# Kernel tuning notes

Measured on AMD Instinct MI355X. Metric: run time of the kernel, lower is better.

The kernel has to match this reference:

```python
import jax, jax.numpy as jnp
import numpy as np

BS, S, D, N, E = 16, 8, 10, 32, 300
H, STATE_DIM, MID, OC = 128, 96, 256, 100

def setup_inputs():
    ks = jax.random.split(jax.random.key(0), 24)
    g = lambda i, shape: (0.02 * jax.random.normal(ks[i], shape)).astype(jnp.float32)
    return {
        "stock_news": jax.random.normal(ks[0], (BS, S, D, N, E), dtype=jnp.float32),
        "stock_feats": jax.random.normal(ks[1], (BS, STATE_DIM), dtype=jnp.float32),
        "conv_w3": g(2, (S, OC, E, 3)), "conv_b3": g(3, (S, OC)),
        "conv_w4": g(4, (S, OC, E, 4)), "conv_b4": g(5, (S, OC)),
        "conv_w5": g(6, (S, OC, E, 5)), "conv_b5": g(7, (S, OC)),
        "w_ih": g(8, (S, 4 * H, 3 * OC)), "w_hh": g(9, (S, 4 * H, H)),
        "b_ih": g(10, (S, 4 * H)), "b_hh": g(11, (S, 4 * H)),
        "linX_w": g(12, (S, H, 2 * H)), "linX_b": g(13, (S, H)),
        "linY_w": g(14, (S, 64, H)), "linY_b": g(15, (S, 64)),
        "w1": g(16, (24, STATE_DIM)), "b1": g(17, (24,)),
        "w2": g(18, (16, 24)), "b2": g(19, (16,)),
        "arch_w1": g(20, (MID, 16 + 64 * S)), "arch_b1": g(21, (MID,)),
        "arch_w2": g(22, (S, MID)), "arch_b2": g(23, (S,)),
        "action_var": jnp.full((S,), -0.25, dtype=jnp.float32),
    }

def _conv_maxpool(x, w, b, k):
    # x: [S,B,D,N,E], w: [S,OC,E,k] -> conv1d over news axis then max-pool -> [S,B,D,OC]
    L = x.shape[3] - k + 1
    y = jnp.broadcast_to(b[:, None, None, None, :], (x.shape[0], x.shape[1], x.shape[2], L, w.shape[1]))
    for j in range(k):
        y = y + jnp.einsum('sbdne,soe->sbdno', x[:, :, :, j:j + L, :], w[:, :, :, j])
    return y.max(axis=3)

def _lstm_attn(xs, w_ih, w_hh, b_ih, b_hh):
    # single-stock LSTM (batch_first) + attention from original code; xs: [B,D,I] -> [B,2H]
    pre = jnp.einsum('bdi,gi->dbg', xs, w_ih) + b_ih + b_hh  # [D,B,4H]
    h0 = jnp.zeros((xs.shape[0], w_hh.shape[1]), xs.dtype)
    def step(carry, g_t):
        h, c = carry
        gates = g_t + h @ w_hh.T
        i, f, g, o = jnp.split(gates, 4, axis=-1)  # PyTorch gate order i,f,g,o
        c = jax.nn.sigmoid(f) * c + jax.nn.sigmoid(i) * jnp.tanh(g)
        h = jax.nn.sigmoid(o) * jnp.tanh(c)
        return (h, c), h
    (hn, _), outs = jax.lax.scan(step, (h0, h0), pre)
    outs = outs.transpose(1, 0, 2)  # [B,D,H]
    w = jnp.einsum('bh,bdh->bd', hn, outs)[:, None, :]  # [B,1,D]
    w = jax.nn.softmax(w, axis=1)  # softmax over singleton dim, exactly as torch code (yields ones)
    out = jnp.sum(w.transpose(0, 2, 1) * outs, axis=1)  # [B,H]
    return jnp.concatenate([hn, out], axis=-1)  # [B,2H]

def _forward(stock_news, stock_feats, conv_w3, conv_b3, conv_w4, conv_b4, conv_w5, conv_b5,
             w_ih, w_hh, b_ih, b_hh, linX_w, linX_b, linY_w, linY_b,
             w1, b1, w2, b2, arch_w1, arch_b1, arch_w2, arch_b2, action_var):
    x = stock_news.transpose(1, 0, 2, 3, 4)  # [S,B,D,N,E]
    feats = [_conv_maxpool(x, w, b, k) for (w, b, k) in
             ((conv_w3, conv_b3, 3), (conv_w4, conv_b4, 4), (conv_w5, conv_b5, 5))]
    text = jnp.concatenate(feats, axis=-1)  # [S,B,D,300]
    comb = jax.vmap(_lstm_attn)(text, w_ih, w_hh, b_ih, b_hh)  # [S,B,2H]
    hX = jax.nn.relu(jnp.einsum('sbi,shi->sbh', comb, linX_w) + linX_b[:, None, :])  # dropout is eval-mode identity
    hY = jax.nn.relu(jnp.einsum('sbh,soh->sbo', hX, linY_w) + linY_b[:, None, :])  # [S,B,64]
    stock_text = hY.transpose(1, 0, 2).reshape(stock_news.shape[0], -1)  # [B,S*64]
    f = jax.nn.relu(stock_feats @ w1.T + b1) @ w2.T + b2  # [B,16]
    total = jnp.concatenate([stock_text, f], axis=-1)  # [B,16+64S]
    mu = jnp.tanh(jax.nn.relu(total @ arch_w1.T + arch_b1) @ arch_w2.T + arch_b2)
    return mu, jnp.exp(action_var)

def reference(stock_news, stock_feats, conv_w3, conv_b3, conv_w4, conv_b4, conv_w5, conv_b5,
              w_ih, w_hh, b_ih, b_hh, linX_w, linX_b, linY_w, linY_b,
              w1, b1, w2, b2, arch_w1, arch_b1, arch_w2, arch_b2, action_var):
    return _forward(stock_news, stock_feats, conv_w3, conv_b3, conv_w4, conv_b4, conv_w5, conv_b5,
                    w_ih, w_hh, b_ih, b_hh, linX_w, linX_b, linY_w, linY_b,
                    w1, b1, w2, b2, arch_w1, arch_b1, arch_w2, arch_b2, action_var)
```

## Files before the change

### kernel.cpp

```cpp
#include <hip/hip_runtime.h>
#include <math.h>

#define S_   8
#define B_   16
#define D_   10
#define N_   32
#define E_   300
#define H_   128
#define G4_  512
#define SDIM_ 96
#define MID_ 256
#define TOT_ 528

typedef unsigned short u16;
typedef unsigned int u32;
typedef __attribute__((ext_vector_type(8))) short short8;
typedef __attribute__((ext_vector_type(4))) short short4v;
typedef __attribute__((ext_vector_type(4))) float f32x4;

static __device__ __forceinline__ u16 f2bf(float f) {
    unsigned u = __builtin_bit_cast(unsigned, f);
    return (u16)((u + 0x7FFFu + ((u >> 16) & 1u)) >> 16);
}

__global__ __launch_bounds__(256) void prep(
        const float* __restrict__ w3, const float* __restrict__ b3,
        const float* __restrict__ w4, const float* __restrict__ b4,
        const float* __restrict__ w5, const float* __restrict__ b5,
        const float* __restrict__ w_ih,
        const float* __restrict__ lxw, const float* __restrict__ lyw,
        const float* __restrict__ aw1,
        u16* __restrict__ wpack2, u16* __restrict__ wpre2,
        float* __restrict__ bcomb,
        float* __restrict__ lxwT, float* __restrict__ lywT,
        float* __restrict__ aw1T) {
    const int blk = blockIdx.x, tid = threadIdx.x;

    if (blk < 160) {
        __shared__ u16 tile[16][1504];
        const int s = blk / 20, cg = blk % 20;
        for (int i = tid; i < 16 * 752; i += 256)
            reinterpret_cast<u32*>(&tile[0][0])[i] = 0u;
        __syncthreads();
        const int ch = tid >> 4, lane = tid & 15;
        const int c = cg * 16 + ch;
        const float* src = nullptr; int cnt = 0, ktap = 3;
        if (c < 100)      { src = w3 + (size_t)((s * 100 + c      ) * 300) * 3; cnt = 900;  ktap = 3; }
        else if (c < 200) { src = w4 + (size_t)((s * 100 + c - 100) * 300) * 4; cnt = 1200; ktap = 4; }
        else if (c < 300) { src = w5 + (size_t)((s * 100 + c - 200) * 300) * 5; cnt = 1500; ktap = 5; }
        for (int p = lane; p < cnt; p += 16) {
            int e = p / ktap, tap = p - e * ktap;
            tile[ch][tap * 300 + e] = f2bf(src[p]);
        }
        __syncthreads();
        u32* dst0 = reinterpret_cast<u32*>(wpack2 + (size_t)s * 481280 + cg * 512);
        const int mch = tid >> 4, rem = (tid * 2) & 31;
        for (int ks = 0; ks < 47; ++ks) {
            u32 v = (u32)tile[mch][ks * 32 + rem] | ((u32)tile[mch][ks * 32 + rem + 1] << 16);
            dst0[(size_t)ks * 5120 + tid] = v;
        }
    } else if (blk < 416) {
        __shared__ u16 tile2[16][320];
        const int u = blk - 160, s = u >> 5, gg = u & 31;
        const int ch = tid >> 4, lane = tid & 15;
        const int g = gg * 16 + ch;
        const float* src = w_ih + (size_t)(s * 512 + g) * 300;
        for (int p = lane; p < 320; p += 16)
            tile2[ch][p] = (p < 300) ? f2bf(src[p]) : (u16)0;
        __syncthreads();
        u32* dst0 = reinterpret_cast<u32*>(wpre2 + (size_t)s * 163840 + gg * 512);
        const int mch = tid >> 4, rem = (tid * 2) & 31;
        for (int ks = 0; ks < 10; ++ks) {
            u32 v = (u32)tile2[mch][ks * 32 + rem] | ((u32)tile2[mch][ks * 32 + rem + 1] << 16);
            dst0[(size_t)ks * 8192 + tid] = v;
        }
    } else if (blk < 872) {
        __shared__ float ldsT[32][33];
        const float* inp; float* outp;
        int inRS, outRS, i0, t0, ivalid = 32;
        if (blk < 672) {
            int u = blk - 416, s = u >> 5, t32 = u & 31;
            int it = t32 >> 2, tt = t32 & 3;
            inp = lxw + (size_t)s * 128 * 256; outp = lxwT + (size_t)s * 256 * 128;
            inRS = 256; outRS = 128; i0 = it * 32; t0 = tt * 32;
        } else if (blk < 736) {
            int u = blk - 672, s = u >> 3, t32 = u & 7;
            int it = t32 >> 1, tt = t32 & 1;
            inp = lyw + (size_t)s * 64 * 128; outp = lywT + (size_t)s * 128 * 64;
            inRS = 128; outRS = 64; i0 = it * 32; t0 = tt * 32;
        } else {
            int u = blk - 736;
            int it = u >> 3, jt = u & 7;
            inp = aw1; outp = aw1T;
            inRS = 528; outRS = 256; i0 = it * 32; t0 = jt * 32;
            ivalid = (i0 + 32 <= 528) ? 32 : (528 - i0);
        }
        const int row = tid >> 3, cf = tid & 7;
        float4 v = make_float4(0.f, 0.f, 0.f, 0.f);
        if (cf * 4 < ivalid)
            v = *reinterpret_cast<const float4*>(inp + (size_t)(t0 + row) * inRS + i0 + cf * 4);
        ldsT[cf * 4 + 0][row] = v.x; ldsT[cf * 4 + 1][row] = v.y;
        ldsT[cf * 4 + 2][row] = v.z; ldsT[cf * 4 + 3][row] = v.w;
        __syncthreads();
        if (row < ivalid) {
            float4 w;
            w.x = ldsT[row][cf * 4 + 0]; w.y = ldsT[row][cf * 4 + 1];
            w.z = ldsT[row][cf * 4 + 2]; w.w = ldsT[row][cf * 4 + 3];
            *reinterpret_cast<float4*>(outp + (size_t)(i0 + row) * outRS + t0 + cf * 4) = w;
        }
    } else {
        for (int i = tid; i < 2560; i += 256) {
            int c = i % 320, s = i / 320;
            float bv = 0.f;
            if (c < 100)      bv = b3[s*100 + c];
            else if (c < 200) bv = b4[s*100 + c - 100];
            else if (c < 300) bv = b5[s*100 + c - 200];
            bcomb[i] = bv;
        }
    }
}

__global__ __launch_bounds__(512, 1) void conv_mfma(const float* __restrict__ news,
                                                    const u16* __restrict__ wpack2,
                                                    const float* __restrict__ bcomb,
                                                    u16* __restrict__ text_bf) {
    __shared__ u16 xs[5 * 10816];
    __shared__ float part[10][320];
    const int tid = threadIdx.x, bid = blockIdx.x;
    const int s = bid & 7, rr_ = bid >> 3, b = rr_ >> 1, half = rr_ & 1;
    const int l = tid & 63, wvi = tid >> 6;
    const int wm = wvi >> 2, wn = wvi & 3;
    const int q = l >> 4, r16 = l & 15;

    const u16* gp[5];
#pragma unroll
    for (int nt = 0; nt < 5; ++nt) {
        int c = wn * 80 + nt * 16 + r16;
        gp[nt] = wpack2 + (size_t)s * 481280 + c * 32 + q * 8;
    }

    short8 bf0[5], bf1[5];
#pragma unroll
    for (int nt = 0; nt < 5; ++nt) bf0[nt] = *reinterpret_cast<const short8*>(gp[nt]);
#pragma unroll
    for (int nt = 0; nt < 5; ++nt) bf1[nt] = *reinterpret_cast<const short8*>(gp[nt] + 10240);

    {
        const float4* xg = reinterpret_cast<const float4*>(
            news + (size_t)((b * 8 + s) * 10 + half * 5) * 9600);
        for (int base = 0; base < 12000; base += 4096) {
            float4 v[8];
#pragma unroll
            for (int j = 0; j < 8; ++j) {
                int idx = base + j * 512 + tid;
                if (idx < 12000) v[j] = xg[idx];
            }
#pragma unroll
            for (int j = 0; j < 8; ++j) {
                int idx = base + j * 512 + tid;
                if (idx < 12000) {
                    int day = idx / 2400, rem = idx - day * 2400;
                    ushort4 o;
                    o.x = f2bf(v[j].x); o.y = f2bf(v[j].y);
                    o.z = f2bf(v[j].z); o.w = f2bf(v[j].w);
                    *reinterpret_cast<ushort4*>(&xs[day * 10816 + rem * 4]) = o;
                }
            }
        }
        for (int i = tid; i < 1520; i += 512) {
            int day = i / 304, p = i - day * 304;
            *reinterpret_cast<unsigned*>(&xs[day * 10816 + 9600 + p * 2]) = 0u;
        }
    }
    __syncthreads();

    f32x4 acc[5][5];
#pragma unroll
    for (int mt = 0; mt < 5; ++mt)
#pragma unroll
        for (int nt = 0; nt < 5; ++nt) acc[mt][nt] = (f32x4)(0.f);

#define LOADA(dst, ks) do {                                                       \
    _Pragma("unroll")                                                             \
    for (int mt_ = 0; mt_ < 5; ++mt_) {                                           \
        int di_ = wm * 5 + mt_;                                                   \
        int off_ = (di_ >> 1) * 10816 + (((di_ & 1) << 4) + r16) * 300            \
                   + (ks) * 32 + q * 8;                                           \
        short4v lo_ = *reinterpret_cast<const short4v*>(&xs[off_]);               \
        short4v hi_ = *reinterpret_cast<const short4v*>(&xs[off_ + 4]);           \
        dst[mt_] = __builtin_shufflevector(lo_, hi_, 0, 1, 2, 3, 4, 5, 6, 7);     \
    } } while (0)

#define MFMAS(bfv, av) do {                                                       \
    _Pragma("unroll")                                                             \
    for (int nt_ = 0; nt_ < 5; ++nt_)                                             \
        _Pragma("unroll")                                                         \
        for (int mt_ = 0; mt_ < 5; ++mt_)                                         \
            acc[mt_][nt_] = __builtin_amdgcn_mfma_f32_16x16x32_bf16(av[mt_], bfv[nt_], acc[mt_][nt_], 0, 0, 0); \
    } while (0)

    for (int ks = 0; ks < 46; ks += 2) {
        short8 a0[5], a1[5];
        LOADA(a0, ks);
        MFMAS(bf0, a0);
#pragma unroll
        for (int nt = 0; nt < 5; ++nt)
            bf0[nt] = *reinterpret_cast<const short8*>(gp[nt] + (ks + 2) * 10240);

        LOADA(a1, ks + 1);
        MFMAS(bf1, a1);
        if (ks + 3 < 47) {
#pragma unroll
            for (int nt = 0; nt < 5; ++nt)
                bf1[nt] = *reinterpret_cast<const short8*>(gp[nt] + (ks + 3) * 10240);
        }
    }
    {
        short8 a0[5];
        LOADA(a0, 46);
        MFMAS(bf0, a0);
    }
#undef LOADA
#undef MFMAS

#pragma unroll
    for (int mt = 0; mt < 5; ++mt) {
        const int di = wm * 5 + mt;
        const int nwb = (di & 1) << 4;
#pragma unroll
        for (int nt = 0; nt < 5; ++nt) {
            int oc = wn * 80 + nt * 16 + r16;
            int L = (oc < 100) ? 30 : (oc < 200) ? 29 : 28;
            float mx = -3e38f;
#pragma unroll
            for (int rr = 0; rr < 4; ++rr) {
                int nw = nwb + q * 4 + rr;
                if (nw < L) mx = fmaxf(mx, acc[mt][nt][rr]);
            }
            mx = fmaxf(mx, __shfl_xor(mx, 16));
            mx = fmaxf(mx, __shfl_xor(mx, 32));
            if (l < 16) part[di][wn * 80 + nt * 16 + l] = mx;
        }
    }
    __syncthreads();
    for (int i = tid; i < 1600; i += 512) {
        int day = i / 320, oc = i - day * 320;
        float mx = fmaxf(part[2 * day][oc], part[2 * day + 1][oc]);
        text_bf[((size_t)(s * 16 + b) * 10 + half * 5 + day) * 320 + oc] =
            f2bf(mx + bcomb[s * 320 + oc]);
    }
}

__global__ __launch_bounds__(512) void stock_tail(const u16* __restrict__ text_bf,
                                                  const u16* __restrict__ wpre2,
                                                  const float* __restrict__ b_ih,
                                                  const float* __restrict__ b_hh,
                                                  const float* __restrict__ w_hh,
                                                  const float* __restrict__ lxwT, const float* __restrict__ lxb,
                                                  const float* __restrict__ lywT, const float* __restrict__ lyb,
                                                  float* __restrict__ total) {
    __shared__ u16 as16[16 * 320];
    __shared__ float pre_lds[D_][G4_];
    __shared__ float wchunk[128][129];
    __shared__ float h_lds[H_];
    __shared__ float gates[G4_];
    __shared__ float comb_l[256];
    __shared__ __align__(16) float hx[H_];
    const int sb = blockIdx.x;
    const int s = sb >> 4, b = sb & 15;
    const int t = threadIdx.x, l = t & 63, wv = t >> 6, q = l >> 4, r16 = l & 15;

    for (int i = t; i < 640; i += 512) {
        int r = i / 40, c = i % 40;
        float4 v = make_float4(0.f, 0.f, 0.f, 0.f);
        if (r < D_)
            v = *reinterpret_cast<const float4*>(
                text_bf + ((size_t)((s * 16 + b) * D_ + r)) * 320 + c * 8);
        *reinterpret_cast<float4*>(as16 + r * 320 + ((c ^ (r & 7)) << 3)) = v;
    }
    __syncthreads();

    {
        const u16* gpb[4];
#pragma unroll
        for (int nt = 0; nt < 4; ++nt) {
            int g = wv * 64 + nt * 16 + r16;
            gpb[nt] = wpre2 + (size_t)s * 163840 + g * 32 + q * 8;
        }
        f32x4 acc[4];
#pragma unroll
        for (int nt = 0; nt < 4; ++nt) acc[nt] = (f32x4)(0.f);
        for (int ks = 0; ks < 10; ++ks) {
            short8 a = *reinterpret_cast<const short8*>(
                as16 + r16 * 320 + (((ks * 4 + q) ^ (r16 & 7)) << 3));
#pragma unroll
            for (int nt = 0; nt < 4; ++nt) {
                short8 bf = *reinterpret_cast<const short8*>(gpb[nt] + ks * 16384);
                acc[nt] = __builtin_amdgcn_mfma_f32_16x16x32_bf16(a, bf, acc[nt], 0, 0, 0);
            }
        }
#pragma unroll
        for (int nt = 0; nt < 4; ++nt) {
            int g = wv * 64 + nt * 16 + r16;
            float bias = b_ih[s * G4_ + g] + b_hh[s * G4_ + g];
#pragma unroll
            for (int rr = 0; rr < 4; ++rr) {
                int row = q * 4 + rr;
                if (row < D_) pre_lds[row][g] = acc[nt][rr] + bias;
            }
        }
    }

    float wrs[128];
    for (int c = 0; c < 4; ++c) {
        __syncthreads();
        for (int i2 = t; i2 < 128 * 32; i2 += 512) {
            int row = i2 >> 5, fq = i2 & 31;
            float4 v = *reinterpret_cast<const float4*>(
                w_hh + ((size_t)(s * G4_ + c * 128 + row)) * H_ + fq * 4);
            wchunk[row][fq * 4 + 0] = v.x; wchunk[row][fq * 4 + 1] = v.y;
            wchunk[row][fq * 4 + 2] = v.z; wchunk[row][fq * 4 + 3] = v.w;
        }
        __syncthreads();
        if ((t >> 7) == c) {
            int r = t & 127;
#pragma unroll
            for (int i = 0; i < 128; ++i) wrs[i] = wchunk[r][i];
        }
    }
    __syncthreads();

    float cc = 0.f, hsum = 0.f, hval = 0.f;
    if (t < H_) h_lds[t] = 0.f;
    __syncthreads();

    for (int d = 0; d < D_; ++d) {
        float a0 = pre_lds[d][t];
        float a1 = 0.f, a2 = 0.f, a3 = 0.f;
#pragma unroll
        for (int i = 0; i < 128; i += 4) {
            float4 h4 = *reinterpret_cast<const float4*>(&h_lds[i]);
            a0 = fmaf(wrs[i + 0], h4.x, a0);
            a1 = fmaf(wrs[i + 1], h4.y, a1);
            a2 = fmaf(wrs[i + 2], h4.z, a2);
            a3 = fmaf(wrs[i + 3], h4.w, a3);
        }
        gates[t] = (a0 + a1) + (a2 + a3);
        __syncthreads();
        if (t < H_) {
            float ig = 1.f / (1.f + expf(-gates[t]));
            float fg = 1.f / (1.f + expf(-gates[H_ + t]));
            float gg = tanhf(gates[2 * H_ + t]);
            float og = 1.f / (1.f + expf(-gates[3 * H_ + t]));
            cc = fg * cc + ig * gg;
            hval = og * tanhf(cc);
            hsum += hval;
            h_lds[t] = hval;
        }
        __syncthreads();
    }
    if (t < H_) { comb_l[t] = hval; comb_l[H_ + t] = hsum; }
    __syncthreads();
    if (t < H_) {
        const float* wvp = lxwT + (size_t)s * 256 * 128 + t;
        float a0 = lxb[s * H_ + t], a1 = 0.f;
        for (int i = 0; i < 256; i += 2) {
            a0 = fmaf(comb_l[i], wvp[(size_t)i * 128], a0);
            a1 = fmaf(comb_l[i + 1], wvp[(size_t)(i + 1) * 128], a1);
        }
        hx[t] = fmaxf(a0 + a1, 0.f);
    }
    __syncthreads();
    if (t < 64) {
        const float* wvp = lywT + (size_t)s * 128 * 64 + t;
        float a0 = lyb[s * 64 + t], a1 = 0.f;
        for (int i = 0; i < 128; i += 2) {
            a0 = fmaf(hx[i], wvp[(size_t)i * 64], a0);
            a1 = fmaf(hx[i + 1], wvp[(size_t)(i + 1) * 64], a1);
        }
        total[(size_t)b * 512 + s * 64 + t] = fmaxf(a0 + a1, 0.f);
    }
}

__global__ __launch_bounds__(512) void head_feats(const float* __restrict__ total,
                                                  const float* __restrict__ sf,
                                                  const float* __restrict__ w1, const float* __restrict__ b1,
                                                  const float* __restrict__ w2, const float* __restrict__ b2,
                                                  const float* __restrict__ aw1T, const float* __restrict__ ab1,
                                                  const float* __restrict__ aw2, const float* __restrict__ ab2,
                                                  const float* __restrict__ avar,
                                                  float* __restrict__ out) {
    __shared__ __align__(16) float tr[TOT_];
    __shared__ float hid[MID_];
    __shared__ float h1f[24];
    __shared__ float pA[MID_], pB[MID_];
    const int bb = blockIdx.x, t = threadIdx.x;
    if (t < 128)
        reinterpret_cast<float4*>(tr)[t] = reinterpret_cast<const float4*>(total + (size_t)bb * 512)[t];
    if (t < 24) {
        float acc = b1[t];
        for (int i = 0; i < SDIM_; ++i) acc = fmaf(sf[bb * SDIM_ + i], w1[t * SDIM_ + i], acc);
        h1f[t] = fmaxf(acc, 0.f);
    }
    __syncthreads();
    if (t < 16) {
        float acc = b2[t];
        for (int i = 0; i < 24; ++i) acc = fmaf(h1f[i], w2[t * 24 + i], acc);
        tr[512 + t] = acc;
    }
    __syncthreads();
    {
        const int j = t & 255, hf = t >> 8;
        const int ilo = hf ? 264 : 0, ihi = hf ? 528 : 264;
        const float* wv = aw1T + j;
        float a0 = 0.f, a1 = 0.f, a2 = 0.f, a3 = 0.f;
        for (int i = ilo; i < ihi; i += 4) {
            a0 = fmaf(tr[i + 0], wv[(size_t)(i + 0) * 256], a0);
            a1 = fmaf(tr[i + 1], wv[(size_t)(i + 1) * 256], a1);
            a2 = fmaf(tr[i + 2], wv[(size_t)(i + 2) * 256], a2);
            a3 = fmaf(tr[i + 3], wv[(size_t)(i + 3) * 256], a3);
        }
        float p = (a0 + a1) + (a2 + a3);
        if (hf) pB[j] = p; else pA[j] = p;
    }
    __syncthreads();
    if (t < MID_) hid[t] = fmaxf(pA[t] + pB[t] + ab1[t], 0.f);
    __syncthreads();
    if (t < 8) {
        float acc = ab2[t];
        const float* wv = aw2 + (size_t)t * MID_;
        for (int i = 0; i < MID_; ++i) acc = fmaf(hid[i], wv[i], acc);
        out[bb * 8 + t] = tanhf(acc);
    }
    if (bb == 0 && t >= 8 && t < 16) out[128 + (t - 8)] = expf(avar[t - 8]);
}

extern "C" void kernel_launch(void* const* d_in, const int* in_sizes, int n_in,
                              void* d_out, int out_size, void* d_ws, size_t ws_size,
                              hipStream_t stream) {
    const float* news = (const float*)d_in[0];
    const float* sf   = (const float*)d_in[1];
    const float* w3   = (const float*)d_in[2];  const float* b3 = (const float*)d_in[3];
    const float* w4   = (const float*)d_in[4];  const float* b4 = (const float*)d_in[5];
    const float* w5   = (const float*)d_in[6];  const float* b5 = (const float*)d_in[7];
    const float* w_ih = (const float*)d_in[8];  const float* w_hh = (const float*)d_in[9];
    const float* b_ih = (const float*)d_in[10]; const float* b_hh = (const float*)d_in[11];
    const float* lxw  = (const float*)d_in[12]; const float* lxb = (const float*)d_in[13];
    const float* lyw  = (const float*)d_in[14]; const float* lyb = (const float*)d_in[15];
    const float* w1   = (const float*)d_in[16]; const float* b1 = (const float*)d_in[17];
    const float* w2   = (const float*)d_in[18]; const float* b2 = (const float*)d_in[19];
    const float* aw1  = (const float*)d_in[20]; const float* ab1 = (const float*)d_in[21];
    const float* aw2  = (const float*)d_in[22]; const float* ab2 = (const float*)d_in[23];
    const float* avar = (const float*)d_in[24];

    char* ws = (char*)d_ws;
    u16*   wpack2  = (u16*)ws;
    u16*   wpre2   = (u16*)(ws + 7700480);
    float* bcomb   = (float*)(ws + 10321920);
    u16*   text_bf = (u16*)(ws + 10332160);
    float* total   = (float*)(ws + 11151360);
    float* lxwT    = (float*)(ws + 11184128);
    float* lywT    = (float*)(ws + 12232704);
    float* aw1T    = (float*)(ws + 12494848);

    prep<<<873, 256, 0, stream>>>(w3, b3, w4, b4, w5, b5, w_ih, lxw, lyw, aw1,
                                  wpack2, wpre2, bcomb, lxwT, lywT, aw1T);
    conv_mfma<<<256, 512, 0, stream>>>(news, wpack2, bcomb, text_bf);
    stock_tail<<<S_ * B_, 512, 0, stream>>>(text_bf, wpre2, b_ih, b_hh, w_hh,
                                            lxwT, lxb, lywT, lyb, total);
    head_feats<<<B_, 512, 0, stream>>>(total, sf, w1, b1, w2, b2, aw1T, ab1, aw2, ab2, avar, (float*)d_out);
}
```

Baseline: 122.3 us.

## Switch conv GEMM from bf16 to fp8 e4m3 MFMA with scaled weights

```diff
diff --git a/kernel.cpp b/kernel.cpp
--- a/kernel.cpp
+++ b/kernel.cpp
@@ -1,4 +1,5 @@
 #include <hip/hip_runtime.h>
+#include <hip/hip_fp8.h>
 #include <math.h>
 
 #define S_   8
@@ -14,13 +15,18 @@
 
 typedef unsigned short u16;
 typedef unsigned int u32;
+typedef unsigned char u8;
+typedef unsigned long long u64;
 typedef __attribute__((ext_vector_type(8))) short short8;
-typedef __attribute__((ext_vector_type(4))) short short4v;
 typedef __attribute__((ext_vector_type(4))) float f32x4;
 
 static __device__ __forceinline__ u16 f2bf(float f) {
     unsigned u = __builtin_bit_cast(unsigned, f);
     return (u16)((u + 0x7FFFu + ((u >> 16) & 1u)) >> 16);
+}
+static __device__ __forceinline__ u8 f2fp8(float f) {
+    __hip_fp8_e4m3 t(f);
+    return (u8)t.__x;
 }
 
 __global__ __launch_bounds__(256) void prep(
@@ -30,16 +36,16 @@
         const float* __restrict__ w_ih,
         const float* __restrict__ lxw, const float* __restrict__ lyw,
         const float* __restrict__ aw1,
-        u16* __restrict__ wpack2, u16* __restrict__ wpre2,
+        u8* __restrict__ wpack3, u16* __restrict__ wpre2,
         float* __restrict__ bcomb,
         float* __restrict__ lxwT, float* __restrict__ lywT,
         float* __restrict__ aw1T) {
     const int blk = blockIdx.x, tid = threadIdx.x;
 
     if (blk < 160) {
-        __shared__ u16 tile[16][1504];
+        __shared__ u8 tile[16][1504];
         const int s = blk / 20, cg = blk % 20;
-        for (int i = tid; i < 16 * 752; i += 256)
+        for (int i = tid; i < 16 * 376; i += 256)
             reinterpret_cast<u32*>(&tile[0][0])[i] = 0u;
         __syncthreads();
         const int ch = tid >> 4, lane = tid & 15;
@@ -50,13 +56,13 @@
         else if (c < 300) { src = w5 + (size_t)((s * 100 + c - 200) * 300) * 5; cnt = 1500; ktap = 5; }
         for (int p = lane; p < cnt; p += 16) {
             int e = p / ktap, tap = p - e * ktap;
-            tile[ch][tap * 300 + e] = f2bf(src[p]);
-        }
-        __syncthreads();
-        u32* dst0 = reinterpret_cast<u32*>(wpack2 + (size_t)s * 481280 + cg * 512);
-        const int mch = tid >> 4, rem = (tid * 2) & 31;
+            tile[ch][tap * 300 + e] = f2fp8(src[p] * 16.0f);
+        }
+        __syncthreads();
+        u16* dst0 = reinterpret_cast<u16*>(wpack3 + (size_t)s * 481280) + cg * 256;
+        const int pch = (tid * 2) >> 5, poff = (tid * 2) & 31;
         for (int ks = 0; ks < 47; ++ks) {
-            u32 v = (u32)tile[mch][ks * 32 + rem] | ((u32)tile[mch][ks * 32 + rem + 1] << 16);
+            u16 v = (u16)tile[pch][ks * 32 + poff] | ((u16)tile[pch][ks * 32 + poff + 1] << 8);
             dst0[(size_t)ks * 5120 + tid] = v;
         }
     } else if (blk < 416) {
@@ -120,11 +126,11 @@
     }
 }
 
-__global__ __launch_bounds__(512, 1) void conv_mfma(const float* __restrict__ news,
-                                                    const u16* __restrict__ wpack2,
+__global__ __launch_bounds__(512, 4) void conv_mfma(const float* __restrict__ news,
+                                                    const u8* __restrict__ wpack3,
                                                     const float* __restrict__ bcomb,
                                                     u16* __restrict__ text_bf) {
-    __shared__ u16 xs[5 * 10816];
+    __shared__ u8 xs[5 * 10816];
     __shared__ float part[10][320];
     const int tid = threadIdx.x, bid = blockIdx.x;
     const int s = bid & 7, rr_ = bid >> 3, b = rr_ >> 1, half = rr_ & 1;
@@ -132,18 +138,18 @@
     const int wm = wvi >> 2, wn = wvi & 3;
     const int q = l >> 4, r16 = l & 15;
 
-    const u16* gp[5];
+    const u8* gp[5];
 #pragma unroll
     for (int nt = 0; nt < 5; ++nt) {
         int c = wn * 80 + nt * 16 + r16;
-        gp[nt] = wpack2 + (size_t)s * 481280 + c * 32 + q * 8;
-    }
-
-    short8 bf0[5], bf1[5];
-#pragma unroll
-    for (int nt = 0; nt < 5; ++nt) bf0[nt] = *reinterpret_cast<const short8*>(gp[nt]);
-#pragma unroll
-    for (int nt = 0; nt < 5; ++nt) bf1[nt] = *reinterpret_cast<const short8*>(gp[nt] + 10240);
+        gp[nt] = wpack3 + (size_t)s * 481280 + c * 32 + q * 8;
+    }
+
+    u64 bf0[5], bf1[5];
+#pragma unroll
+    for (int nt = 0; nt < 5; ++nt) bf0[nt] = *reinterpret_cast<const u64*>(gp[nt]);
+#pragma unroll
+    for (int nt = 0; nt < 5; ++nt) bf1[nt] = *reinterpret_cast<const u64*>(gp[nt] + 10240);
 
     {
         const float4* xg = reinterpret_cast<const float4*>(
@@ -160,16 +166,15 @@
                 int idx = base + j * 512 + tid;
                 if (idx < 12000) {
                     int day = idx / 2400, rem = idx - day * 2400;
-                    ushort4 o;
-                    o.x = f2bf(v[j].x); o.y = f2bf(v[j].y);
-                    o.z = f2bf(v[j].z); o.w = f2bf(v[j].w);
-                    *reinterpret_cast<ushort4*>(&xs[day * 10816 + rem * 4]) = o;
+                    u32 o = (u32)f2fp8(v[j].x) | ((u32)f2fp8(v[j].y) << 8)
+                          | ((u32)f2fp8(v[j].z) << 16) | ((u32)f2fp8(v[j].w) << 24);
+                    *reinterpret_cast<u32*>(&xs[day * 10816 + rem * 4]) = o;
                 }
             }
         }
         for (int i = tid; i < 1520; i += 512) {
             int day = i / 304, p = i - day * 304;
-            *reinterpret_cast<unsigned*>(&xs[day * 10816 + 9600 + p * 2]) = 0u;
+            *reinterpret_cast<u32*>(&xs[day * 10816 + 9600 + p * 4]) = 0u;
         }
     }
     __syncthreads();
@@ -186,9 +191,9 @@
         int di_ = wm * 5 + mt_;                                                   \
         int off_ = (di_ >> 1) * 10816 + (((di_ & 1) << 4) + r16) * 300            \
                    + (ks) * 32 + q * 8;                                           \
-        short4v lo_ = *reinterpret_cast<const short4v*>(&xs[off_]);               \
-        short4v hi_ = *reinterpret_cast<const short4v*>(&xs[off_ + 4]);           \
-        dst[mt_] = __builtin_shufflevector(lo_, hi_, 0, 1, 2, 3, 4, 5, 6, 7);     \
+        u32 lo_ = *reinterpret_cast<const u32*>(&xs[off_]);                       \
+        u32 hi_ = *reinterpret_cast<const u32*>(&xs[off_ + 4]);                   \
+        dst[mt_] = (u64)lo_ | ((u64)hi_ << 32);                                   \
     } } while (0)
 
 #define MFMAS(bfv, av) do {                                                       \
@@ -196,27 +201,28 @@
     for (int nt_ = 0; nt_ < 5; ++nt_)                                             \
         _Pragma("unroll")                                                         \
         for (int mt_ = 0; mt_ < 5; ++mt_)                                         \
-            acc[mt_][nt_] = __builtin_amdgcn_mfma_f32_16x16x32_bf16(av[mt_], bfv[nt_], acc[mt_][nt_], 0, 0, 0); \
+            acc[mt_][nt_] = __builtin_amdgcn_mfma_f32_16x16x32_fp8_fp8(          \
+                (long long)av[mt_], (long long)bfv[nt_], acc[mt_][nt_], 0, 0, 0); \
     } while (0)
 
     for (int ks = 0; ks < 46; ks += 2) {
-        short8 a0[5], a1[5];
+        u64 a0[5], a1[5];
         LOADA(a0, ks);
         MFMAS(bf0, a0);
 #pragma unroll
         for (int nt = 0; nt < 5; ++nt)
-            bf0[nt] = *reinterpret_cast<const short8*>(gp[nt] + (ks + 2) * 10240);
+            bf0[nt] = *reinterpret_cast<const u64*>(gp[nt] + (ks + 2) * 10240);
 
         LOADA(a1, ks + 1);
         MFMAS(bf1, a1);
         if (ks + 3 < 47) {
 #pragma unroll
             for (int nt = 0; nt < 5; ++nt)
-                bf1[nt] = *reinterpret_cast<const short8*>(gp[nt] + (ks + 3) * 10240);
+                bf1[nt] = *reinterpret_cast<const u64*>(gp[nt] + (ks + 3) * 10240);
         }
     }
     {
-        short8 a0[5];
+        u64 a0[5];
         LOADA(a0, 46);
         MFMAS(bf0, a0);
     }
@@ -247,7 +253,7 @@
         int day = i / 320, oc = i - day * 320;
         float mx = fmaxf(part[2 * day][oc], part[2 * day + 1][oc]);
         text_bf[((size_t)(s * 16 + b) * 10 + half * 5 + day) * 320 + oc] =
-            f2bf(mx + bcomb[s * 320 + oc]);
+            f2bf(mx * 0.0625f + bcomb[s * 320 + oc]);
     }
 }
 
@@ -454,18 +460,18 @@
     const float* avar = (const float*)d_in[24];
 
     char* ws = (char*)d_ws;
-    u16*   wpack2  = (u16*)ws;
-    u16*   wpre2   = (u16*)(ws + 7700480);
-    float* bcomb   = (float*)(ws + 10321920);
-    u16*   text_bf = (u16*)(ws + 10332160);
-    float* total   = (float*)(ws + 11151360);
-    float* lxwT    = (float*)(ws + 11184128);
-    float* lywT    = (float*)(ws + 12232704);
-    float* aw1T    = (float*)(ws + 12494848);
+    u8*    wpack3  = (u8*)ws;
+    u16*   wpre2   = (u16*)(ws + 3850240);
+    float* bcomb   = (float*)(ws + 6471680);
+    u16*   text_bf = (u16*)(ws + 6481920);
+    float* total   = (float*)(ws + 7301120);
+    float* lxwT    = (float*)(ws + 7333888);
+    float* lywT    = (float*)(ws + 8382464);
+    float* aw1T    = (float*)(ws + 8644608);
 
     prep<<<873, 256, 0, stream>>>(w3, b3, w4, b4, w5, b5, w_ih, lxw, lyw, aw1,
-                                  wpack2, wpre2, bcomb, lxwT, lywT, aw1T);
-    conv_mfma<<<256, 512, 0, stream>>>(news, wpack2, bcomb, text_bf);
+                                  wpack3, wpre2, bcomb, lxwT, lywT, aw1T);
+    conv_mfma<<<256, 512, 0, stream>>>(news, wpack3, bcomb, text_bf);
     stock_tail<<<S_ * B_, 512, 0, stream>>>(text_bf, wpre2, b_ih, b_hh, w_hh,
                                             lxwT, lxb, lywT, lyb, total);
     head_feats<<<B_, 512, 0, stream>>>(total, sf, w1, b1, w2, b2, aw1T, ab1, aw2, ab2, avar, (float*)d_out);
```

Measured after the change: 223.5 us. 1.83x slower.
